# Kernel tuning notes

Measured on AMD Instinct MI355X. Metric: run time of the kernel, lower is better.

The kernel has to match this reference:

```python
import jax, jax.numpy as jnp
import numpy as np

EPS = 1e-6
AREA_WIDTH = 3
NHEAD = 8
DIM = 16


def _skew(v):
    # v: [N,3] -> [N,3,3] cross-product matrix
    x, y, z = v[..., 0], v[..., 1], v[..., 2]
    zero = jnp.zeros_like(x)
    return jnp.stack([
        jnp.stack([zero, -z, y], -1),
        jnp.stack([z, zero, -x], -1),
        jnp.stack([-y, x, zero], -1)], -2)


def _create_meshgrid(h, w):
    # kornia create_meshgrid(..., normalized=False): last dim is (x, y), row-major flatten
    xs = jnp.arange(w, dtype=jnp.float32)
    ys = jnp.arange(h, dtype=jnp.float32)
    gx, gy = jnp.meshgrid(xs, ys, indexing='xy')  # [h,w]
    return jnp.stack([gx, gy], -1).reshape(h * w, 2)  # [S,2]


def _epipolar_lines(coord, R, t, K0, K1):
    # coord [S,2]; R [N,3,3]; t [N,3,1] -> lines [N,S,3] (unit-normalized a,b), mode [N,S]
    S = coord.shape[0]
    p = jnp.concatenate([coord, jnp.ones((S, 1), coord.dtype)], -1)  # [S,3]
    E = _skew(t[..., 0]) @ R                                         # [t]_x R
    F = jnp.swapaxes(jnp.linalg.inv(K1), -1, -2) @ E @ jnp.linalg.inv(K0)
    lines = jnp.einsum('nij,sj->nsi', F, p)
    n = jnp.linalg.norm(lines[..., :2], axis=-1, keepdims=True)
    lines = lines / jnp.maximum(n, 1e-12)
    mode = jnp.abs(lines[..., 1]) >= jnp.abs(lines[..., 0])  # True: solve y(x) (|b|>=|a|)
    return lines, mode


def _get_mask(lines, mode, coord, area_width):
    # lines [N,L,3], mode [N,L], coord [S,2] -> within [N,L,S]
    a, b, c = lines[..., 0], lines[..., 1], lines[..., 2]
    xs, ys = coord[:, 0], coord[:, 1]
    hw = area_width / 2.0
    safe = lambda d: jnp.where(jnp.abs(d) < 1e-12, 1e-12, d)
    cy = (-a / safe(b))[..., None] * xs + (-c / safe(b))[..., None]  # [N,L,S]
    cx = (-b / safe(a))[..., None] * ys + (-c / safe(a))[..., None]
    wy = (ys < cy + hw) & (ys > cy - hw)
    wx = (xs < cx + hw) & (xs > cx - hw)
    return jnp.where(mode[..., None], wy, wx)


def _gather_index(within, C):
    # sort-based top-C compaction, index 0 doubles as padding (faithful to source)
    S = within.shape[-1]
    idx = jnp.arange(S, dtype=jnp.int32)
    ti = jnp.where(within, idx[None, None, :], 0)
    ti = jnp.sort(ti, axis=-1)[..., -C:]
    return ti, ti != 0


def _feature_map(x):
    return jax.nn.elu(x) + 1.0


def reference(queries, keys, values, solved_sample, K0, K1, R, t, h0c, w0c, scale):
    N, L, H, D = queries.shape
    sol = np.asarray(solved_sample).astype(bool)  # static split of the batch
    sol_idx = np.nonzero(sol)[0]
    uns_idx = np.nonzero(~sol)[0]
    Q = _feature_map(queries)
    K = _feature_map(keys)
    out = jnp.zeros((N, L, H, D), queries.dtype)

    if sol_idx.size > 0:  # epipolar-gathered candidate attention, direction '0to1'
        coord = _create_meshgrid(h0c, w0c)
        K0s = K0[sol_idx].at[:, :2, :].mul(1.0 / scale)
        K1s = K1[sol_idx].at[:, :2, :].mul(1.0 / scale)
        C = max(h0c, w0c) * AREA_WIDTH
        lines, mode = _epipolar_lines(coord, R[sol_idx], t[sol_idx], K0s, K1s)
        within = _get_mask(lines, mode, coord, AREA_WIDTH)       # [Ns,L,S]
        index, mask = _gather_index(within, C)                    # [Ns,L,C]
        Ns = sol_idx.size
        n_ix = jnp.arange(Ns)[:, None, None]
        Qs = Q[sol_idx]
        Ks = K[sol_idx][n_ix, index]            # [Ns,L,C,H,D]
        Vs = values[sol_idx][n_ix, index]
        m = mask[..., None, None].astype(Ks.dtype)
        Ks = Ks * m
        Vs = Vs * m / C
        KV = jnp.einsum('nlchd,nlchv->nlhdv', Ks, Vs)
        Z = 1.0 / (jnp.einsum('nlhd,nlhd->nlh', Qs, Ks.sum(2)) + EPS)
        out = out.at[sol_idx].set(jnp.einsum('nlhd,nlhdv,nlh->nlhv', Qs, KV, Z) * C)

    if uns_idx.size > 0:  # plain linear attention
        Qu, Ku, Vu = Q[uns_idx], K[uns_idx], values[uns_idx]
        S = Ku.shape[1]
        KV = jnp.einsum('nshd,nshv->nhdv', Ku, Vu / S)
        Z = 1.0 / (jnp.einsum('nlhd,nhd->nlh', Qu, Ku.sum(1)) + EPS)
        out = out.at[uns_idx].set(jnp.einsum('nlhd,nhdv,nlh->nlhv', Qu, KV, Z) * S)
    return out


def setup_inputs() -> dict:
    key = jax.random.key(0)
    kq, kk, kv = jax.random.split(key, 3)
    N, H, D = 4, NHEAD, DIM
    h0c, w0c = 48, 64
    L = h0c * w0c
    queries = jax.random.normal(kq, (N, L, H, D), jnp.float32)
    keys = jax.random.normal(kk, (N, L, H, D), jnp.float32)
    values = jax.random.normal(kv, (N, L, H, D), jnp.float32)
    solved_sample = jnp.array([True, True, False, False])
    Kmat = np.array([[600., 0., 256.], [0., 600., 192.], [0., 0., 1.]], np.float32)
    K0 = jnp.asarray(np.tile(Kmat, (N, 1, 1)))
    Rl, tl = [], []
    for i in range(N):
        th = 0.05 * (i + 1)
        Rl.append(np.array([[np.cos(th), 0., np.sin(th)], [0., 1., 0.],
                            [-np.sin(th), 0., np.cos(th)]], np.float32))
        tl.append(np.array([[0.2 + 0.01 * i], [0.05], [0.02]], np.float32))
    R = jnp.asarray(np.stack(Rl))
    t = jnp.asarray(np.stack(tl))
    return {"queries": queries, "keys": keys, "values": values,
            "solved_sample": solved_sample, "K0": K0, "K1": K0, "R": R, "t": t,
            "h0c": h0c, "w0c": w0c, "scale": 8}
```

## Files before the change

kernel.cpp:

```cpp
#include <hip/hip_runtime.h>
#include <math.h>

#define NHEAD 8
#define DIM   16
#define EPSF  1e-6f
#define KVCH  8

typedef _Float16 half2_t __attribute__((ext_vector_type(2)));
typedef _Float16 half4_t __attribute__((ext_vector_type(4)));
typedef _Float16 half8_t __attribute__((ext_vector_type(8)));

#if defined(__has_builtin)
#if __has_builtin(__builtin_amdgcn_fdot2)
#define HAVE_FDOT2 1
#endif
#endif

__device__ __forceinline__ float dot2(half2_t a, half2_t b, float c) {
#ifdef HAVE_FDOT2
    return __builtin_amdgcn_fdot2(a, b, c, false);
#else
    return c + (float)a.x * (float)b.x + (float)a.y * (float)b.y;
#endif
}

__device__ __forceinline__ bool solved_flag(const void* p, int i) {
    const unsigned int* u = (const unsigned int*)p;
    unsigned int v0 = u[0];
    if (v0 <= 1u)             return u[i] != 0u;
    if (v0 == 0x3F800000u)    return ((const float*)p)[i] != 0.0f;
    return ((const unsigned char*)p)[i] != 0;
}

__device__ __forceinline__ float fm(float x) {
    return x > 0.f ? x + 1.f : expf(x);
}

__device__ void inv3d(const double* M, double* inv) {
    double det = M[0]*(M[4]*M[8]-M[5]*M[7]) - M[1]*(M[3]*M[8]-M[5]*M[6]) + M[2]*(M[3]*M[7]-M[4]*M[6]);
    double id = 1.0 / det;
    inv[0] =  (M[4]*M[8]-M[5]*M[7])*id;
    inv[1] = -(M[1]*M[8]-M[2]*M[7])*id;
    inv[2] =  (M[1]*M[5]-M[2]*M[4])*id;
    inv[3] = -(M[3]*M[8]-M[5]*M[6])*id;
    inv[4] =  (M[0]*M[8]-M[2]*M[6])*id;
    inv[5] = -(M[0]*M[5]-M[2]*M[3])*id;
    inv[6] =  (M[3]*M[7]-M[4]*M[6])*id;
    inv[7] = -(M[0]*M[7]-M[1]*M[6])*id;
    inv[8] =  (M[0]*M[4]-M[1]*M[3])*id;
}

__device__ void compute_F_one(const float* K0, const float* K1, const float* R,
                              const float* t, float invs, float* Fout, int n) {
    double A[9], B[9];
    for (int i = 0; i < 9; ++i) {
        float a = K0[n*9 + i], b = K1[n*9 + i];
        if (i < 6) { a *= invs; b *= invs; }
        A[i] = (double)a; B[i] = (double)b;
    }
    double iA[9], iB[9];
    inv3d(A, iA); inv3d(B, iB);
    double tx = t[n*3+0], ty = t[n*3+1], tz = t[n*3+2];
    double S[9] = {0.0,-tz,ty, tz,0.0,-tx, -ty,tx,0.0};
    double E[9], M[9];
    for (int i = 0; i < 3; ++i)
        for (int j = 0; j < 3; ++j) {
            double s = 0.0;
            for (int k = 0; k < 3; ++k) s += S[i*3+k] * (double)R[n*9 + k*3 + j];
            E[i*3+j] = s;
        }
    for (int i = 0; i < 3; ++i)
        for (int j = 0; j < 3; ++j) {
            double s = 0.0;
            for (int k = 0; k < 3; ++k) s += E[i*3+k] * iA[k*3+j];
            M[i*3+j] = s;
        }
    for (int i = 0; i < 3; ++i)
        for (int j = 0; j < 3; ++j) {
            double s = 0.0;
            for (int k = 0; k < 3; ++k) s += iB[k*3+i] * M[k*3+j];
            Fout[n*9 + i*3 + j] = (float)s;
        }
}

__launch_bounds__(256)
__global__ void prep_kv(const float4* __restrict__ Kr4, const float4* __restrict__ Vr4,
                        _Float16* __restrict__ Kh, _Float16* __restrict__ Vh, int n4,
                        const float* __restrict__ Kr, const float* __restrict__ Vr,
                        const void* __restrict__ flags,
                        float* __restrict__ KVp, float* __restrict__ Ksp,
                        const float* __restrict__ K0, const float* __restrict__ K1,
                        const float* __restrict__ R,  const float* __restrict__ t,
                        const int* __restrict__ scale_p, float* __restrict__ Fout,
                        int N, int L, int PB) {
    if ((int)blockIdx.x < PB) {
        int i = blockIdx.x * 256 + threadIdx.x;
        if (i < n4) {
            float4 k = Kr4[i];
            half4_t kh = { (_Float16)fm(k.x), (_Float16)fm(k.y), (_Float16)fm(k.z), (_Float16)fm(k.w) };
            ((half4_t*)Kh)[i] = kh;
            float4 v = Vr4[i];
            half4_t vh = { (_Float16)v.x, (_Float16)v.y, (_Float16)v.z, (_Float16)v.w };
            ((half4_t*)Vh)[i] = vh;
        }
        if (blockIdx.x == 0 && threadIdx.x < (unsigned)N) {
            float invs = 1.0f / (float)(*scale_p);
            compute_F_one(K0, K1, R, t, invs, Fout, threadIdx.x);
        }
    } else {
        int kb = blockIdx.x - PB;
        int chunk = kb & (KVCH - 1);
        int h = (kb >> 3) & 7;
        int n = kb >> 6;
        if (n >= N || solved_flag(flags, n)) return;
        int tdx = threadIdx.x;
        int d = tdx >> 4, v = tdx & 15;
        int rowsPer = (L + KVCH - 1) / KVCH;
        int r0 = chunk * rowsPer;
        int r1 = min(r0 + rowsPer, L);
        const float* Kb = Kr + (size_t)n * L * (NHEAD * DIM) + h * DIM;
        const float* Vb = Vr + (size_t)n * L * (NHEAD * DIM) + h * DIM;
        float acc = 0.f, ks = 0.f;
        #pragma unroll 8
        for (int s = r0; s < r1; ++s) {
            float kd = fm(Kb[(size_t)s * (NHEAD * DIM) + d]);
            float vv = Vb[(size_t)s * (NHEAD * DIM) + v];
            acc += kd * vv;
            ks  += kd;
        }
        KVp[(((size_t)chunk * N + n) * NHEAD + h) * 256 + (d << 4) + v] = acc;
        if (v == 0) Ksp[(((size_t)chunk * N + n) * NHEAD + h) * 16 + d] = ks;
    }
}

__launch_bounds__(256)
__global__ void mega(const float* __restrict__ Qr,
                     const _Float16* __restrict__ Kh, const _Float16* __restrict__ Vh,
                     const void* __restrict__ flags,  const float* __restrict__ F,
                     const float* __restrict__ KVp,   const float* __restrict__ Ksp,
                     float* __restrict__ outp,
                     const int* __restrict__ h0c_p, const int* __restrict__ w0c_p,
                     int N, int L, int Bs) {
    if ((int)blockIdx.x < Bs) {
        int wid = (blockIdx.x << 2) | (threadIdx.x >> 6);
        wid = __builtin_amdgcn_readfirstlane(wid);
        int lane = threadIdx.x & 63;
        int n = wid / L;
        if (n >= N) return;
        if (!solved_flag(flags, n)) return;
        int s = wid - n * L;
        int W  = *w0c_p;
        int Hc = *h0c_p;
        float px = (float)(s % W);
        float py = (float)(s / W);

        const float* Fn = F + n * 9;
        float a = Fn[0]*px + Fn[1]*py + Fn[2];
        float b = Fn[3]*px + Fn[4]*py + Fn[5];
        float c = Fn[6]*px + Fn[7]*py + Fn[8];
        float nrm = sqrtf(a*a + b*b);
        float mdiv = fmaxf(nrm, 1e-12f);
        a /= mdiv; b /= mdiv; c /= mdiv;
        bool mode = fabsf(b) >= fabsf(a);

        float slope, inter;
        int outerN, innerMax, sI, sO;
        if (mode) {
            float bs = (fabsf(b) < 1e-12f) ? 1e-12f : b;
            slope = -a / bs; inter = -c / bs;
            outerN = W; innerMax = Hc; sI = W; sO = 1;
        } else {
            float as = (fabsf(a) < 1e-12f) ? 1e-12f : a;
            slope = -b / as; inter = -c / as;
            outerN = Hc; innerMax = W; sI = 1; sO = W;
        }

        int c8 = lane >> 3;
        int h  = lane & 7;

        const float4* q4 = (const float4*)(Qr + (size_t)wid * (NHEAD * DIM) + h * DIM);
        half2_t q2[8];
        {
            float4 a0 = q4[0], a1 = q4[1], a2 = q4[2], a3 = q4[3];
            q2[0] = (half2_t){ (_Float16)fm(a0.x), (_Float16)fm(a0.y) };
            q2[1] = (half2_t){ (_Float16)fm(a0.z), (_Float16)fm(a0.w) };
            q2[2] = (half2_t){ (_Float16)fm(a1.x), (_Float16)fm(a1.y) };
            q2[3] = (half2_t){ (_Float16)fm(a1.z), (_Float16)fm(a1.w) };
            q2[4] = (half2_t){ (_Float16)fm(a2.x), (_Float16)fm(a2.y) };
            q2[5] = (half2_t){ (_Float16)fm(a2.z), (_Float16)fm(a2.w) };
            q2[6] = (half2_t){ (_Float16)fm(a3.x), (_Float16)fm(a3.y) };
            q2[7] = (half2_t){ (_Float16)fm(a3.z), (_Float16)fm(a3.w) };
        }

        const _Float16* Kb = Kh + (size_t)n * L * (NHEAD * DIM);
        const _Float16* Vb = Vh + (size_t)n * L * (NHEAD * DIM);

        half2_t acc2[8];
        #pragma unroll
        for (int i = 0; i < 8; ++i) acc2[i] = (half2_t){ (_Float16)0.f, (_Float16)0.f };
        float den = 0.f;

        int totalC = outerN * 3;
        int groups = (totalC + 7) >> 3;
        const float hw = 1.5f;

        #pragma unroll 2
        for (int g = 0; g < groups; ++g) {
            int m = (g << 3) + c8;
            int o = (int)((unsigned)m / 3u);
            int j = m - o * 3;
            float cc = fmaf(slope, (float)o, inter);
            float lo = cc - hw, hi = cc + hw;
            int ii = (int)floorf(lo) + 1 + j;
            float fi = (float)ii;
            bool valid = (m < totalC) && (ii >= 0) && (ii < innerMax)
                         && (fi > lo) && (fi < hi);
            int s2 = ii * sI + o * sO;
            valid = valid && (s2 != 0);
            int idx = ((valid ? s2 : 0) << 7) + (h << 4);
            const half8_t* kr = (const half8_t*)(Kb + idx);
            const half8_t* vr = (const half8_t*)(Vb + idx);
            half8_t k0 = kr[0], k1 = kr[1];
            half8_t v0 = vr[0], v1 = vr[1];
            union H8 { half8_t v; half2_t h[4]; };
            H8 ku0, ku1, vu0, vu1;
            ku0.v = k0; ku1.v = k1; vu0.v = v0; vu1.v = v1;
            float sA = 0.f, sB = 0.f;
            sA = dot2(q2[0], ku0.h[0], sA);
            sB = dot2(q2[1], ku0.h[1], sB);
            sA = dot2(q2[2], ku0.h[2], sA);
            sB = dot2(q2[3], ku0.h[3], sB);
            sA = dot2(q2[4], ku1.h[0], sA);
            sB = dot2(q2[5], ku1.h[1], sB);
            sA = dot2(q2[6], ku1.h[2], sA);
            sB = dot2(q2[7], ku1.h[3], sB);
            float sc = sA + sB;
            sc = valid ? sc : 0.f;
            den += sc;
            _Float16 sch = (_Float16)sc;
            half2_t scv = (half2_t){ sch, sch };
            acc2[0] += scv * vu0.h[0];
            acc2[1] += scv * vu0.h[1];
            acc2[2] += scv * vu0.h[2];
            acc2[3] += scv * vu0.h[3];
            acc2[4] += scv * vu1.h[0];
            acc2[5] += scv * vu1.h[1];
            acc2[6] += scv * vu1.h[2];
            acc2[7] += scv * vu1.h[3];
        }

        den += __shfl_xor(den, 8);
        den += __shfl_xor(den, 16);
        den += __shfl_xor(den, 32);

        bool hi8 = (lane & 8) != 0;
        half2_t t4[4];
        #pragma unroll
        for (int j2 = 0; j2 < 4; ++j2) {
            half2_t send = hi8 ? acc2[j2] : acc2[4 + j2];
            int rr = __shfl_xor(__builtin_bit_cast(int, send), 8);
            half2_t keep = hi8 ? acc2[4 + j2] : acc2[j2];
            t4[j2] = keep + __builtin_bit_cast(half2_t, rr);
        }
        bool hi16 = (lane & 16) != 0;
        half2_t t2[2];
        #pragma unroll
        for (int j2 = 0; j2 < 2; ++j2) {
            half2_t send = hi16 ? t4[j2] : t4[2 + j2];
            int rr = __shfl_xor(__builtin_bit_cast(int, send), 16);
            half2_t keep = hi16 ? t4[2 + j2] : t4[j2];
            t2[j2] = keep + __builtin_bit_cast(half2_t, rr);
        }
        bool hi32 = (lane & 32) != 0;
        half2_t t1;
        {
            half2_t send = hi32 ? t2[0] : t2[1];
            int rr = __shfl_xor(__builtin_bit_cast(int, send), 32);
            half2_t keep = hi32 ? t2[1] : t2[0];
            t1 = keep + __builtin_bit_cast(half2_t, rr);
        }
        int e0 = (hi8 ? 8 : 0) + (hi16 ? 4 : 0) + (hi32 ? 2 : 0);
        float r = 1.0f / (den + EPSF);
        float2 o2 = { (float)t1.x * r, (float)t1.y * r };
        *(float2*)(outp + (size_t)wid * (NHEAD * DIM) + h * DIM + e0) = o2;
    } else {
        long long tot2 = (long long)N * L * NHEAD * DIM / 2;
        long long idx2 = (long long)(blockIdx.x - Bs) * 256 + threadIdx.x;
        if (idx2 >= tot2) return;
        int p = (int)(idx2 & 63);
        int h = p >> 3;
        int v = (p & 7) * 2;
        long long ns = idx2 >> 6;
        int n = (int)(ns / L);
        if (solved_flag(flags, n)) return;
        const float* qrow = Qr + ns * (NHEAD * DIM) + h * DIM;
        float num0 = 0.f, num1 = 0.f, den = 0.f;
        #pragma unroll
        for (int d = 0; d < 16; ++d) {
            float qd = fm(qrow[d]);
            #pragma unroll
            for (int cch = 0; cch < KVCH; ++cch) {
                const float2 kv2 = *(const float2*)(KVp + (((size_t)cch * N + n) * NHEAD + h) * 256 + (d << 4) + v);
                num0 += qd * kv2.x;
                num1 += qd * kv2.y;
                den  += qd * Ksp[(((size_t)cch * N + n) * NHEAD + h) * 16 + d] * (1.0f / 16.0f);
            }
        }
        den *= 16.0f;
        float rdiv = 1.0f / (den + EPSF);
        size_t ob = ns * (NHEAD * DIM) + h * DIM + v;
        outp[ob]     = num0 * rdiv;
        outp[ob + 1] = num1 * rdiv;
    }
}

extern "C" void kernel_launch(void* const* d_in, const int* in_sizes, int n_in,
                              void* d_out, int out_size, void* d_ws, size_t ws_size,
                              hipStream_t stream) {
    const float* Qr   = (const float*)d_in[0];
    const float* Kr   = (const float*)d_in[1];
    const float* Vr   = (const float*)d_in[2];
    const void*  flag = d_in[3];
    const float* K0   = (const float*)d_in[4];
    const float* K1   = (const float*)d_in[5];
    const float* R    = (const float*)d_in[6];
    const float* t    = (const float*)d_in[7];
    const int*   h0c  = (const int*)d_in[8];
    const int*   w0c  = (const int*)d_in[9];
    const int*   scl  = (const int*)d_in[10];

    int N = in_sizes[3];
    int T = in_sizes[0];
    int L = T / (N * NHEAD * DIM);

    _Float16* Kh = (_Float16*)d_ws;
    _Float16* Vh = Kh + T;
    float* Fm   = (float*)(Vh + T);
    float* KVp  = Fm + (size_t)N * 9;
    float* Ksp  = KVp + (size_t)KVCH * N * NHEAD * 256;

    float* outp = (float*)d_out;

    int n4 = T / 4;
    int PB = (n4 + 255) / 256;
    int KB = N * NHEAD * KVCH;
    prep_kv<<<PB + KB, 256, 0, stream>>>((const float4*)Kr, (const float4*)Vr,
                                         Kh, Vh, n4, Kr, Vr, flag, KVp, Ksp,
                                         K0, K1, R, t, scl, Fm, N, L, PB);

    int Bs = (N * L + 3) / 4;
    long long tot2 = (long long)N * L * NHEAD * DIM / 2;
    int Bu = (int)((tot2 + 255) / 256);
    mega<<<Bs + Bu, 256, 0, stream>>>(Qr, Kh, Vh, flag, Fm, KVp, Ksp, outp,
                                      h0c, w0c, N, L, Bs);
}
```

Measured before the change: 173.7 us.

## Interleave fp16 K/V rows and software-pipeline gathers with fp32 accumulation

The prep pass now packs each position's fp16 K and V into one interleaved 512-byte row, so a single gather pulls both from adjacent memory. The sparse epipolar attention loop is restructured so each lane handles half a head-dim for two heads. It uses a three-buffer rotation that issues the next candidate's loads before consuming the current one, which hides gather latency. Accumulation moves from packed fp16 to fp32, with a pairwise shuffle for the dot product and a plain butterfly reduction at the end. This costs more registers and shuffles per candidate in exchange for better memory-level parallelism and accuracy.

```diff
diff --git a/kernel.cpp b/kernel.cpp
--- a/kernel.cpp
+++ b/kernel.cpp
@@ -8,7 +8,6 @@
 
 typedef _Float16 half2_t __attribute__((ext_vector_type(2)));
 typedef _Float16 half4_t __attribute__((ext_vector_type(4)));
-typedef _Float16 half8_t __attribute__((ext_vector_type(8)));
 
 #if defined(__has_builtin)
 #if __has_builtin(__builtin_amdgcn_fdot2)
@@ -85,7 +84,7 @@
 
 __launch_bounds__(256)
 __global__ void prep_kv(const float4* __restrict__ Kr4, const float4* __restrict__ Vr4,
-                        _Float16* __restrict__ Kh, _Float16* __restrict__ Vh, int n4,
+                        _Float16* __restrict__ KVh, int n4,
                         const float* __restrict__ Kr, const float* __restrict__ Vr,
                         const void* __restrict__ flags,
                         float* __restrict__ KVp, float* __restrict__ Ksp,
@@ -97,11 +96,13 @@
         int i = blockIdx.x * 256 + threadIdx.x;
         if (i < n4) {
             float4 k = Kr4[i];
+            float4 v = Vr4[i];
             half4_t kh = { (_Float16)fm(k.x), (_Float16)fm(k.y), (_Float16)fm(k.z), (_Float16)fm(k.w) };
-            ((half4_t*)Kh)[i] = kh;
-            float4 v = Vr4[i];
             half4_t vh = { (_Float16)v.x, (_Float16)v.y, (_Float16)v.z, (_Float16)v.w };
-            ((half4_t*)Vh)[i] = vh;
+            int r = i >> 5;
+            int w = (i & 31) << 2;
+            *(half4_t*)(KVh + (size_t)r * 256 + w)       = kh;
+            *(half4_t*)(KVh + (size_t)r * 256 + 128 + w) = vh;
         }
         if (blockIdx.x == 0 && threadIdx.x < (unsigned)N) {
             float invs = 1.0f / (float)(*scale_p);
@@ -133,9 +134,59 @@
     }
 }
 
+struct Buf {
+    uint4 kl, kh, vl, vh;
+    float msk;
+};
+union H16 { uint4 u; half2_t h[4]; _Float16 e[8]; };
+
+__device__ __forceinline__ void issue(Buf& b, const char* KVb, int base16,
+                                      float slope, float inter, int oo, float c1,
+                                      int ob, int outerN, int innerMax, int sI, int sO) {
+    int io = ob + oo;
+    float fo = (float)io;
+    float cc = fmaf(slope, fo, inter);
+    float lo = cc - 1.5f;
+    float fl = floorf(lo);
+    float fi = fl + c1;
+    int ii = (int)fi;
+    bool val = (io < outerN) & (ii >= 0) & (ii < innerMax) & (fi > lo) & (fi < cc + 1.5f);
+    int s2 = ii * sI + io * sO;
+    val = val && (s2 != 0);
+    int off = ((val ? s2 : 0) << 9) + base16;
+    const char* p = KVb + off;
+    b.kl = *(const uint4*)(p);
+    b.kh = *(const uint4*)(p + 128);
+    b.vl = *(const uint4*)(p + 256);
+    b.vh = *(const uint4*)(p + 384);
+    b.msk = val ? 1.f : 0.f;
+}
+
+__device__ __forceinline__ void consume(const Buf& b, const half2_t* ql, const half2_t* qh,
+                                        float* aL, float* aH, float& dL, float& dH) {
+    H16 k0, k1, v0, v1;
+    k0.u = b.kl; k1.u = b.kh; v0.u = b.vl; v1.u = b.vh;
+    float sA = 0.f, sB = 0.f;
+    #pragma unroll
+    for (int i = 0; i < 4; ++i) {
+        sA = dot2(ql[i], k0.h[i], sA);
+        sB = dot2(qh[i], k1.h[i], sB);
+    }
+    sA += __shfl_xor(sA, 1);
+    sB += __shfl_xor(sB, 1);
+    float scL = sA * b.msk;
+    float scH = sB * b.msk;
+    dL += scL; dH += scH;
+    #pragma unroll
+    for (int i = 0; i < 8; ++i) {
+        aL[i] = fmaf(scL, (float)v0.e[i], aL[i]);
+        aH[i] = fmaf(scH, (float)v1.e[i], aH[i]);
+    }
+}
+
 __launch_bounds__(256)
 __global__ void mega(const float* __restrict__ Qr,
-                     const _Float16* __restrict__ Kh, const _Float16* __restrict__ Vh,
+                     const _Float16* __restrict__ KVh,
                      const void* __restrict__ flags,  const float* __restrict__ F,
                      const float* __restrict__ KVp,   const float* __restrict__ Ksp,
                      float* __restrict__ outp,
@@ -175,114 +226,89 @@
             outerN = Hc; innerMax = W; sI = 1; sO = W;
         }
 
-        int c8 = lane >> 3;
-        int h  = lane & 7;
-
-        const float4* q4 = (const float4*)(Qr + (size_t)wid * (NHEAD * DIM) + h * DIM);
-        half2_t q2[8];
+        int cL  = lane >> 3;
+        int sub = lane & 7;
+        int hL  = sub >> 1;
+        int dh  = sub & 1;
+        int base16 = sub << 4;
+
+        const float* qbase = Qr + (size_t)wid * (NHEAD * DIM);
+        half2_t ql[4], qh[4];
         {
-            float4 a0 = q4[0], a1 = q4[1], a2 = q4[2], a3 = q4[3];
-            q2[0] = (half2_t){ (_Float16)fm(a0.x), (_Float16)fm(a0.y) };
-            q2[1] = (half2_t){ (_Float16)fm(a0.z), (_Float16)fm(a0.w) };
-            q2[2] = (half2_t){ (_Float16)fm(a1.x), (_Float16)fm(a1.y) };
-            q2[3] = (half2_t){ (_Float16)fm(a1.z), (_Float16)fm(a1.w) };
-            q2[4] = (half2_t){ (_Float16)fm(a2.x), (_Float16)fm(a2.y) };
-            q2[5] = (half2_t){ (_Float16)fm(a2.z), (_Float16)fm(a2.w) };
-            q2[6] = (half2_t){ (_Float16)fm(a3.x), (_Float16)fm(a3.y) };
-            q2[7] = (half2_t){ (_Float16)fm(a3.z), (_Float16)fm(a3.w) };
-        }
-
-        const _Float16* Kb = Kh + (size_t)n * L * (NHEAD * DIM);
-        const _Float16* Vb = Vh + (size_t)n * L * (NHEAD * DIM);
-
-        half2_t acc2[8];
+            const float4* qa = (const float4*)(qbase + hL * DIM + dh * 8);
+            float4 a0 = qa[0], a1 = qa[1];
+            ql[0] = (half2_t){ (_Float16)fm(a0.x), (_Float16)fm(a0.y) };
+            ql[1] = (half2_t){ (_Float16)fm(a0.z), (_Float16)fm(a0.w) };
+            ql[2] = (half2_t){ (_Float16)fm(a1.x), (_Float16)fm(a1.y) };
+            ql[3] = (half2_t){ (_Float16)fm(a1.z), (_Float16)fm(a1.w) };
+            const float4* qb = (const float4*)(qbase + (hL + 4) * DIM + dh * 8);
+            float4 b0 = qb[0], b1 = qb[1];
+            qh[0] = (half2_t){ (_Float16)fm(b0.x), (_Float16)fm(b0.y) };
+            qh[1] = (half2_t){ (_Float16)fm(b0.z), (_Float16)fm(b0.w) };
+            qh[2] = (half2_t){ (_Float16)fm(b1.x), (_Float16)fm(b1.y) };
+            qh[3] = (half2_t){ (_Float16)fm(b1.z), (_Float16)fm(b1.w) };
+        }
+
+        const char* KVb = (const char*)KVh + (size_t)n * L * 512;
+
+        int mm0 = cL, mm1 = 8 + cL, mm2 = 16 + cL;
+        int oo0 = mm0 / 3, oo1 = mm1 / 3, oo2 = mm2 / 3;
+        float c10 = (float)(1 + (mm0 - 3 * oo0));
+        float c11 = (float)(1 + (mm1 - 3 * oo1));
+        float c12 = (float)(1 + (mm2 - 3 * oo2));
+
+        int totalC = outerN * 3;
+        int NM3 = (totalC + 23) / 24;
+
+        float accL[8], accH[8];
         #pragma unroll
-        for (int i = 0; i < 8; ++i) acc2[i] = (half2_t){ (_Float16)0.f, (_Float16)0.f };
-        float den = 0.f;
-
-        int totalC = outerN * 3;
-        int groups = (totalC + 7) >> 3;
-        const float hw = 1.5f;
-
-        #pragma unroll 2
-        for (int g = 0; g < groups; ++g) {
-            int m = (g << 3) + c8;
-            int o = (int)((unsigned)m / 3u);
-            int j = m - o * 3;
-            float cc = fmaf(slope, (float)o, inter);
-            float lo = cc - hw, hi = cc + hw;
-            int ii = (int)floorf(lo) + 1 + j;
-            float fi = (float)ii;
-            bool valid = (m < totalC) && (ii >= 0) && (ii < innerMax)
-                         && (fi > lo) && (fi < hi);
-            int s2 = ii * sI + o * sO;
-            valid = valid && (s2 != 0);
-            int idx = ((valid ? s2 : 0) << 7) + (h << 4);
-            const half8_t* kr = (const half8_t*)(Kb + idx);
-            const half8_t* vr = (const half8_t*)(Vb + idx);
-            half8_t k0 = kr[0], k1 = kr[1];
-            half8_t v0 = vr[0], v1 = vr[1];
-            union H8 { half8_t v; half2_t h[4]; };
-            H8 ku0, ku1, vu0, vu1;
-            ku0.v = k0; ku1.v = k1; vu0.v = v0; vu1.v = v1;
-            float sA = 0.f, sB = 0.f;
-            sA = dot2(q2[0], ku0.h[0], sA);
-            sB = dot2(q2[1], ku0.h[1], sB);
-            sA = dot2(q2[2], ku0.h[2], sA);
-            sB = dot2(q2[3], ku0.h[3], sB);
-            sA = dot2(q2[4], ku1.h[0], sA);
-            sB = dot2(q2[5], ku1.h[1], sB);
-            sA = dot2(q2[6], ku1.h[2], sA);
-            sB = dot2(q2[7], ku1.h[3], sB);
-            float sc = sA + sB;
-            sc = valid ? sc : 0.f;
-            den += sc;
-            _Float16 sch = (_Float16)sc;
-            half2_t scv = (half2_t){ sch, sch };
-            acc2[0] += scv * vu0.h[0];
-            acc2[1] += scv * vu0.h[1];
-            acc2[2] += scv * vu0.h[2];
-            acc2[3] += scv * vu0.h[3];
-            acc2[4] += scv * vu1.h[0];
-            acc2[5] += scv * vu1.h[1];
-            acc2[6] += scv * vu1.h[2];
-            acc2[7] += scv * vu1.h[3];
-        }
-
-        den += __shfl_xor(den, 8);
-        den += __shfl_xor(den, 16);
-        den += __shfl_xor(den, 32);
-
-        bool hi8 = (lane & 8) != 0;
-        half2_t t4[4];
+        for (int i = 0; i < 8; ++i) { accL[i] = 0.f; accH[i] = 0.f; }
+        float denL = 0.f, denH = 0.f;
+
+        Buf A, B, C;
+        issue(A, KVb, base16, slope, inter, oo0, c10, 0, outerN, innerMax, sI, sO);
+        issue(B, KVb, base16, slope, inter, oo1, c11, 0, outerN, innerMax, sI, sO);
+        int ob = 0;
+        for (int k = 0; k < NM3; ++k) {
+            issue(C, KVb, base16, slope, inter, oo2, c12, ob, outerN, innerMax, sI, sO);
+            consume(A, ql, qh, accL, accH, denL, denH);
+            int obn = ob + 8;
+            issue(A, KVb, base16, slope, inter, oo0, c10, obn, outerN, innerMax, sI, sO);
+            consume(B, ql, qh, accL, accH, denL, denH);
+            issue(B, KVb, base16, slope, inter, oo1, c11, obn, outerN, innerMax, sI, sO);
+            consume(C, ql, qh, accL, accH, denL, denH);
+            ob = obn;
+        }
+
         #pragma unroll
-        for (int j2 = 0; j2 < 4; ++j2) {
-            half2_t send = hi8 ? acc2[j2] : acc2[4 + j2];
-            int rr = __shfl_xor(__builtin_bit_cast(int, send), 8);
-            half2_t keep = hi8 ? acc2[4 + j2] : acc2[j2];
-            t4[j2] = keep + __builtin_bit_cast(half2_t, rr);
-        }
-        bool hi16 = (lane & 16) != 0;
-        half2_t t2[2];
-        #pragma unroll
-        for (int j2 = 0; j2 < 2; ++j2) {
-            half2_t send = hi16 ? t4[j2] : t4[2 + j2];
-            int rr = __shfl_xor(__builtin_bit_cast(int, send), 16);
-            half2_t keep = hi16 ? t4[2 + j2] : t4[j2];
-            t2[j2] = keep + __builtin_bit_cast(half2_t, rr);
-        }
-        bool hi32 = (lane & 32) != 0;
-        half2_t t1;
-        {
-            half2_t send = hi32 ? t2[0] : t2[1];
-            int rr = __shfl_xor(__builtin_bit_cast(int, send), 32);
-            half2_t keep = hi32 ? t2[1] : t2[0];
-            t1 = keep + __builtin_bit_cast(half2_t, rr);
-        }
-        int e0 = (hi8 ? 8 : 0) + (hi16 ? 4 : 0) + (hi32 ? 2 : 0);
-        float r = 1.0f / (den + EPSF);
-        float2 o2 = { (float)t1.x * r, (float)t1.y * r };
-        *(float2*)(outp + (size_t)wid * (NHEAD * DIM) + h * DIM + e0) = o2;
+        for (int j = 0; j < 8; ++j) {
+            accL[j] += __shfl_xor(accL[j], 8);
+            accL[j] += __shfl_xor(accL[j], 16);
+            accL[j] += __shfl_xor(accL[j], 32);
+            accH[j] += __shfl_xor(accH[j], 8);
+            accH[j] += __shfl_xor(accH[j], 16);
+            accH[j] += __shfl_xor(accH[j], 32);
+        }
+        denL += __shfl_xor(denL, 8);
+        denL += __shfl_xor(denL, 16);
+        denL += __shfl_xor(denL, 32);
+        denH += __shfl_xor(denH, 8);
+        denH += __shfl_xor(denH, 16);
+        denH += __shfl_xor(denH, 32);
+
+        if (lane < 8) {
+            float rL = 1.0f / (denL + EPSF);
+            float rH = 1.0f / (denH + EPSF);
+            float* op = outp + (size_t)wid * (NHEAD * DIM) + lane * 8;
+            float4 o0 = { accL[0]*rL, accL[1]*rL, accL[2]*rL, accL[3]*rL };
+            float4 o1 = { accL[4]*rL, accL[5]*rL, accL[6]*rL, accL[7]*rL };
+            ((float4*)op)[0] = o0;
+            ((float4*)op)[1] = o1;
+            float4 o2 = { accH[0]*rH, accH[1]*rH, accH[2]*rH, accH[3]*rH };
+            float4 o3 = { accH[4]*rH, accH[5]*rH, accH[6]*rH, accH[7]*rH };
+            ((float4*)(op + 64))[0] = o2;
+            ((float4*)(op + 64))[1] = o3;
+        }
     } else {
         long long tot2 = (long long)N * L * NHEAD * DIM / 2;
         long long idx2 = (long long)(blockIdx.x - Bs) * 256 + threadIdx.x;
@@ -333,9 +359,8 @@
     int T = in_sizes[0];
     int L = T / (N * NHEAD * DIM);
 
-    _Float16* Kh = (_Float16*)d_ws;
-    _Float16* Vh = Kh + T;
-    float* Fm   = (float*)(Vh + T);
+    _Float16* KVh = (_Float16*)d_ws;
+    float* Fm   = (float*)(KVh + (size_t)2 * T);
     float* KVp  = Fm + (size_t)N * 9;
     float* Ksp  = KVp + (size_t)KVCH * N * NHEAD * 256;
 
@@ -345,12 +370,12 @@
     int PB = (n4 + 255) / 256;
     int KB = N * NHEAD * KVCH;
     prep_kv<<<PB + KB, 256, 0, stream>>>((const float4*)Kr, (const float4*)Vr,
-                                         Kh, Vh, n4, Kr, Vr, flag, KVp, Ksp,
+                                         KVh, n4, Kr, Vr, flag, KVp, Ksp,
                                          K0, K1, R, t, scl, Fm, N, L, PB);
 
     int Bs = (N * L + 3) / 4;
     long long tot2 = (long long)N * L * NHEAD * DIM / 2;
     int Bu = (int)((tot2 + 255) / 256);
-    mega<<<Bs + Bu, 256, 0, stream>>>(Qr, Kh, Vh, flag, Fm, KVp, Ksp, outp,
+    mega<<<Bs + Bu, 256, 0, stream>>>(Qr, KVh, flag, Fm, KVp, Ksp, outp,
                                       h0c, w0c, N, L, Bs);
 }
```

Result: no change. 173.4 us (-0.2%).
